# Kernel tuning notes

Hardware: AMD Instinct MI355X
Metric: run time of the kernel (lower is better)

## Reference

```python
import jax, jax.numpy as jnp
import numpy as np

B, T, P, K, R, M = 32, 2048, 128, 256, 8, 64
TAU, TAU_X, TAU_Z = 5, 100.0, 100.0


def _mlp(x, layers):
    # torch nn.Linear: y = x @ W.T + b, each followed by tanh
    for W, b in layers:
        x = jnp.tanh(x @ W.T + b)
    return x


def setup_inputs() -> dict:
    key = jax.random.key(0)
    ks = jax.random.split(key, 24)
    g = lambda k, shp, s=0.1: (jax.random.normal(k, shp, dtype=jnp.float32) * s)
    inp = {
        "in_seq": jax.random.normal(ks[0], (B, T, P), dtype=jnp.float32),
        "L": g(ks[1], (K, R)),
        "Rm": g(ks[2], (K, R)),
        "Wz": g(ks[3], (M, M)),
        "Az_w": g(ks[4], (R, M)),
        "Az_b": jnp.zeros((R,), jnp.float32),
        "ex1_w": g(ks[5], (K, P)), "ex1_b": jnp.zeros((K,), jnp.float32),
        "ex2_w": g(ks[6], (K, K)), "ex2_b": jnp.zeros((K,), jnp.float32),
        "ex3_w": g(ks[7], (K, K)), "ex3_b": jnp.zeros((K,), jnp.float32),
        "ez1_w": g(ks[8], (M, P)), "ez1_b": jnp.zeros((M,), jnp.float32),
        "ez2_w": g(ks[9], (M, M)), "ez2_b": jnp.zeros((M,), jnp.float32),
        "ez3_w": g(ks[10], (M, M)), "ez3_b": jnp.zeros((M,), jnp.float32),
        "de1_w": g(ks[11], (K, K)), "de1_b": jnp.zeros((K,), jnp.float32),
        "de2_w": g(ks[12], (P, K)), "de2_b": jnp.zeros((P,), jnp.float32),
    }
    return inp


def reference(in_seq, L, Rm, Wz, Az_w, Az_b,
              ex1_w, ex1_b, ex2_w, ex2_b, ex3_w, ex3_b,
              ez1_w, ez1_b, ez2_w, ez2_b, ez3_w, ez3_b,
              de1_w, de1_b, de2_w, de2_b):
    enc_x = [(ex1_w, ex1_b), (ex2_w, ex2_b), (ex3_w, ex3_b)]
    enc_z = [(ez1_w, ez1_b), (ez2_w, ez2_b), (ez3_w, ez3_b)]
    dec = [(de1_w, de1_b), (de2_w, de2_b)]

    x_seq = _mlp(in_seq, enc_x)  # [B,T,K]
    z_seq = _mlp(in_seq, enc_z)  # [B,T,M]

    def step(carry, inp):
        x, z = carry          # [B,K], [B,M]
        t, xt, zt = inp       # scalar, [B,K], [B,M]
        # teacher forcing reset every TAU steps (not at t=0)
        reset = (t % TAU == 0) & (t > 0)
        x = jnp.where(reset, xt, x)
        z = jnp.where(reset, zt, z)
        # neuromodulator dynamics
        dz = -z + jnp.tanh(z) @ Wz.T
        z = z + dz / TAU_Z
        s = jax.nn.sigmoid(z @ Az_w.T + Az_b)  # [B,R]
        # low-rank recurrence: bmm(tanh(x), einsum('bir,jr,kr->bijk',s,L,R)[:,0])
        # == ((tanh(x) @ L) * s) @ R.T   (same math, O(K*R) per element)
        dx = -x + ((jnp.tanh(x) @ L) * s) @ Rm.T
        x = x + dx / TAU_X
        x_dec = _mlp(x, dec)  # [B,P]
        return (x, z), (x_dec, z)

    x0 = x_seq[:, 0, :]
    z0 = z_seq[:, 0, :]
    ts = jnp.arange(T)
    xs = jnp.swapaxes(x_seq, 0, 1)  # [T,B,K]
    zs = jnp.swapaxes(z_seq, 0, 1)  # [T,B,M]
    _, (x_pred_t, z_pred_t) = jax.lax.scan(step, (x0, z0), (ts, xs, zs))
    x_pred = jnp.swapaxes(x_pred_t, 0, 1)  # [B,T,P]
    z_pred = jnp.swapaxes(z_pred_t, 0, 1)  # [B,T,M]

    x_recon = _mlp(x_seq, dec)  # [B,T,P]
    return (x_pred, x_recon, z_pred, z_seq)
```

## Files before the change

kernel.cpp:

```cpp
#include <hip/hip_runtime.h>
#include <math.h>

constexpr int B = 32, T = 2048, P = 128, K = 256, R = 8, M = 64;
constexpr int BT = B * T;
constexpr int TAU = 5;
constexpr int NSEG = (T + TAU - 1) / TAU;
constexpr float INV_TAU_X = 1.0f / 100.0f;
constexpr float INV_TAU_Z = 1.0f / 100.0f;

typedef short bf16x4 __attribute__((ext_vector_type(4)));
typedef short bf16x8 __attribute__((ext_vector_type(8)));
typedef float f32x4 __attribute__((ext_vector_type(4)));

static __device__ __forceinline__ short f2bf(float f) {
  unsigned u = __builtin_bit_cast(unsigned, f);
  u += 0x7FFF + ((u >> 16) & 1);
  return (short)(u >> 16);
}
static __device__ __forceinline__ float bf2f(short h) {
  unsigned u = ((unsigned)(unsigned short)h) << 16;
  return __builtin_bit_cast(float, u);
}

static __device__ __forceinline__ float tanh_fast(float x) {
  const float e = __expf(2.f * x);
  return 1.f - 2.f * __builtin_amdgcn_rcpf(e + 1.f);
}
static __device__ __forceinline__ float sigmoid_fast(float x) {
  return __builtin_amdgcn_rcpf(1.f + __expf(-x));
}

static __device__ __forceinline__ void async16(const void* g, void* l) {
  __builtin_amdgcn_global_load_lds(
      (const __attribute__((address_space(1))) void*)g,
      (__attribute__((address_space(3))) void*)l, 16, 0, 0);
}

template <int CTRL>
static __device__ __forceinline__ float dppadd(float p) {
  return p + __builtin_bit_cast(
                 float, __builtin_amdgcn_update_dpp(
                            0, __builtin_bit_cast(int, p), CTRL, 0xF, 0xF, true));
}

static __device__ __forceinline__ void allreduce8(float p[R]) {
#pragma unroll
  for (int r = 0; r < R; ++r) p[r] = dppadd<0xB1>(p[r]);
#pragma unroll
  for (int r = 0; r < R; ++r) p[r] = dppadd<0x4E>(p[r]);
#pragma unroll
  for (int r = 0; r < R; ++r) p[r] = dppadd<0x141>(p[r]);
#pragma unroll
  for (int r = 0; r < R; ++r) p[r] = dppadd<0x140>(p[r]);
#pragma unroll
  for (int r = 0; r < R; ++r)
    p[r] += __builtin_bit_cast(float, __builtin_amdgcn_ds_swizzle(
                                          __builtin_bit_cast(int, p[r]), 0x401F));
#pragma unroll
  for (int r = 0; r < R; ++r)
    p[r] += __shfl_xor(p[r], 32, 64);
}

__global__ __launch_bounds__(256) void split_kernel(
    const float* __restrict__ in, short* __restrict__ h,
    short* __restrict__ l, int n4) {
  const int i = blockIdx.x * 256 + threadIdx.x;
  if (i >= n4) return;
  const float4 v = ((const float4*)in)[i];
  const float f[4] = {v.x, v.y, v.z, v.w};
  bf16x4 ph, pl;
#pragma unroll
  for (int q = 0; q < 4; ++q) {
    ph[q] = f2bf(f[q]);
    pl[q] = f2bf(f[q] - bf2f(ph[q]));
  }
  ((bf16x4*)h)[i] = ph;
  ((bf16x4*)l)[i] = pl;
}

struct W8 {
  const float* src[8];
  unsigned hoff[8];
  unsigned n4[8];
};
__global__ __launch_bounds__(256) void split8_kernel(W8 p, short* __restrict__ dst) {
  const int w = blockIdx.y;
  const int i = blockIdx.x * 256 + threadIdx.x;
  if (i >= (int)p.n4[w]) return;
  const float4 v = ((const float4*)p.src[w])[i];
  const float f[4] = {v.x, v.y, v.z, v.w};
  bf16x4 ph, pl;
#pragma unroll
  for (int q = 0; q < 4; ++q) {
    ph[q] = f2bf(f[q]);
    pl[q] = f2bf(f[q] - bf2f(ph[q]));
  }
  *(bf16x4*)&dst[p.hoff[w] + i * 4] = ph;
  *(bf16x4*)&dst[p.hoff[w] + p.n4[w] * 4 + i * 4] = pl;
}

template <int KIN, int KOUT, int BN, bool SPLIT_OUT>
__global__ __launch_bounds__(256) void gemm_mfma(
    const short* __restrict__ Ah, const short* __restrict__ Al,
    const short* __restrict__ Bh, const short* __restrict__ Bl,
    const float* __restrict__ bias,
    short* __restrict__ Ch, short* __restrict__ Cl,
    float* __restrict__ Cf) {
  constexpr int BK = 64;
  constexpr int WNT = BN / 32;
  constexpr int NB = BN / 8;
  static_assert(KIN % BK == 0, "K tiling");

  __shared__ short AsH[128 * BK];
  __shared__ short AsL[128 * BK];
  __shared__ short BsH[BN * BK];
  __shared__ short BsL[BN * BK];

  const int tid = threadIdx.x;
  const int wave = tid >> 6, lane = tid & 63;
  const int l16 = lane & 15, quad = lane >> 4;
  const int sw = l16 & 7;
  const int warpM = wave & 1, warpN = wave >> 1;
  const int row0 = blockIdx.x * 128;
  const int col0 = blockIdx.y * BN;
  const int srow = lane >> 3;
  const int schunk = (lane & 7) ^ srow;

  f32x4 acc[4][WNT];
#pragma unroll
  for (int i = 0; i < 4; ++i)
#pragma unroll
    for (int j = 0; j < WNT; ++j) acc[i][j] = (f32x4){0.f, 0.f, 0.f, 0.f};

  for (int k0 = 0; k0 < KIN; k0 += BK) {
#pragma unroll
    for (int t = wave; t < 16; t += 4) {
      const size_t goff = (size_t)(row0 + t * 8 + srow) * KIN + k0 + schunk * 8;
      async16(&Ah[goff], &AsH[t * 512]);
      async16(&Al[goff], &AsL[t * 512]);
    }
#pragma unroll
    for (int t = wave; t < NB; t += 4) {
      const size_t goff = (size_t)(col0 + t * 8 + srow) * KIN + k0 + schunk * 8;
      async16(&Bh[goff], &BsH[t * 512]);
      async16(&Bl[goff], &BsL[t * 512]);
    }
    __syncthreads();

#pragma unroll
    for (int kk = 0; kk < 2; ++kk) {
      const int qc = kk * 4 + quad;
      const int qs = (qc ^ sw) * 8;
      bf16x8 ah[4], al[4], bh[WNT], bl[WNT];
#pragma unroll
      for (int i = 0; i < 4; ++i) {
        const int off = (warpM * 64 + i * 16 + l16) * BK + qs;
        ah[i] = *(const bf16x8*)&AsH[off];
        al[i] = *(const bf16x8*)&AsL[off];
      }
#pragma unroll
      for (int j = 0; j < WNT; ++j) {
        const int off = (warpN * WNT * 16 + j * 16 + l16) * BK + qs;
        bh[j] = *(const bf16x8*)&BsH[off];
        bl[j] = *(const bf16x8*)&BsL[off];
      }
#pragma unroll
      for (int i = 0; i < 4; ++i)
#pragma unroll
        for (int j = 0; j < WNT; ++j) {
          acc[i][j] = __builtin_amdgcn_mfma_f32_16x16x32_bf16(ah[i], bh[j],
                                                              acc[i][j], 0, 0, 0);
          acc[i][j] = __builtin_amdgcn_mfma_f32_16x16x32_bf16(al[i], bh[j],
                                                              acc[i][j], 0, 0, 0);
          acc[i][j] = __builtin_amdgcn_mfma_f32_16x16x32_bf16(ah[i], bl[j],
                                                              acc[i][j], 0, 0, 0);
        }
    }
    __syncthreads();
  }

#pragma unroll
  for (int j = 0; j < WNT; ++j) {
    const int col = col0 + warpN * WNT * 16 + j * 16 + l16;
    const float bj = bias[col];
#pragma unroll
    for (int i = 0; i < 4; ++i) {
      const int rbase = row0 + warpM * 64 + i * 16 + quad * 4;
#pragma unroll
      for (int r = 0; r < 4; ++r) {
        const float v = tanh_fast(acc[i][j][r] + bj);
        const size_t idx = (size_t)(rbase + r) * KOUT + col;
        if (SPLIT_OUT) {
          const short h = f2bf(v);
          Ch[idx] = h;
          Cl[idx] = f2bf(v - bf2f(h));
        } else {
          Cf[idx] = v;
        }
      }
    }
  }
}

__global__ __launch_bounds__(512) void scan_kernel(
    const short* xh, const short* xl,
    const float* __restrict__ z_seq,
    const float* __restrict__ Lm, const float* __restrict__ Rm,
    const float* __restrict__ Wz, const float* __restrict__ Az_w,
    const float* __restrict__ Az_b,
    short* xsh, short* xsl,
    float* __restrict__ z_pred) {
  __shared__ __align__(16) float Wz_s[M][68];
  __shared__ __align__(16) float Ls[K * R];
  __shared__ __align__(16) float Rs[K * R];
  __shared__ __align__(16) float tz_s[8][M];

  const int tid = threadIdx.x;
  for (int i = tid; i < M * M; i += 512) Wz_s[i >> 6][i & 63] = Wz[i];
  ((float4*)Ls)[tid] = ((const float4*)Lm)[tid];
  ((float4*)Rs)[tid] = ((const float4*)Rm)[tid];
  __syncthreads();

  const int wave = tid >> 6;
  const int lane = tid & 63;
  const int chain = blockIdx.x * 8 + wave;
  const int b = chain / NSEG;
  const int seg = chain % NSEG;
  const int t0 = seg * TAU;

  float azw[R], azb[R];
#pragma unroll
  for (int r = 0; r < R; ++r) {
    azw[r] = Az_w[r * M + lane];
    azb[r] = Az_b[r];
  }

  float x[4], z;
  {
    const size_t base = ((size_t)b * T + t0);
#pragma unroll
    for (int j = 0; j < 4; ++j)
      x[j] = bf2f(xh[base * K + lane + 64 * j]) + bf2f(xl[base * K + lane + 64 * j]);
    z = z_seq[base * M + lane];
  }

  const float4* wrow = (const float4*)&Wz_s[lane][0];
  const float4* trow = (const float4*)&tz_s[wave][0];

  for (int tt = 0; tt < TAU; ++tt) {
    const int t = t0 + tt;
    const float tz = tanh_fast(z);
    tz_s[wave][lane] = tz;
    float zacc = 0.f;
#pragma unroll
    for (int j = 0; j < 16; ++j) {
      const float4 w = wrow[j], tv = trow[j];
      zacc += w.x * tv.x + w.y * tv.y + w.z * tv.z + w.w * tv.w;
    }
    const float znew = z + (zacc - z) * INV_TAU_Z;

    float s[R];
#pragma unroll
    for (int r = 0; r < R; ++r) s[r] = znew * azw[r];
    allreduce8(s);
#pragma unroll
    for (int r = 0; r < R; ++r) s[r] = sigmoid_fast(s[r] + azb[r]);

    float tx4[4];
#pragma unroll
    for (int j = 0; j < 4; ++j) tx4[j] = tanh_fast(x[j]);
    float v[R];
#pragma unroll
    for (int r = 0; r < R; ++r) v[r] = 0.f;
#pragma unroll
    for (int j = 0; j < 4; ++j) {
      const int kb = (lane + 64 * j) * 8;
      const f32x4 la = *(const f32x4*)&Ls[kb];
      const f32x4 lb = *(const f32x4*)&Ls[kb + 4];
      const float txj = tx4[j];
      v[0] += txj * la[0]; v[1] += txj * la[1];
      v[2] += txj * la[2]; v[3] += txj * la[3];
      v[4] += txj * lb[0]; v[5] += txj * lb[1];
      v[6] += txj * lb[2]; v[7] += txj * lb[3];
    }
    allreduce8(v);
#pragma unroll
    for (int r = 0; r < R; ++r) v[r] *= s[r];
#pragma unroll
    for (int j = 0; j < 4; ++j) {
      const int kb = (lane + 64 * j) * 8;
      const f32x4 ra = *(const f32x4*)&Rs[kb];
      const f32x4 rb = *(const f32x4*)&Rs[kb + 4];
      const float xacc = v[0] * ra[0] + v[1] * ra[1] + v[2] * ra[2] +
                         v[3] * ra[3] + v[4] * rb[0] + v[5] * rb[1] +
                         v[6] * rb[2] + v[7] * rb[3];
      x[j] = x[j] + (xacc - x[j]) * INV_TAU_X;
    }

    if (t < T) {
      const size_t o = ((size_t)b * T + t);
#pragma unroll
      for (int j = 0; j < 4; ++j) {
        const short h = f2bf(x[j]);
        xsh[o * K + lane + 64 * j] = h;
        xsl[o * K + lane + 64 * j] = f2bf(x[j] - bf2f(h));
      }
      z_pred[o * M + lane] = znew;
    }
    z = znew;
  }
}

extern "C" void kernel_launch(void* const* d_in, const int* in_sizes, int n_in,
                              void* d_out, int out_size, void* d_ws,
                              size_t ws_size, hipStream_t stream) {
  const float* in_seq = (const float*)d_in[0];
  const float* Lm    = (const float*)d_in[1];
  const float* Rm    = (const float*)d_in[2];
  const float* Wz    = (const float*)d_in[3];
  const float* Az_w  = (const float*)d_in[4];
  const float* Az_b  = (const float*)d_in[5];
  const float* ex1_w = (const float*)d_in[6];
  const float* ex1_b = (const float*)d_in[7];
  const float* ex2_w = (const float*)d_in[8];
  const float* ex2_b = (const float*)d_in[9];
  const float* ex3_w = (const float*)d_in[10];
  const float* ex3_b = (const float*)d_in[11];
  const float* ez1_w = (const float*)d_in[12];
  const float* ez1_b = (const float*)d_in[13];
  const float* ez2_w = (const float*)d_in[14];
  const float* ez2_b = (const float*)d_in[15];
  const float* ez3_w = (const float*)d_in[16];
  const float* ez3_b = (const float*)d_in[17];
  const float* de1_w = (const float*)d_in[18];
  const float* de1_b = (const float*)d_in[19];
  const float* de2_w = (const float*)d_in[20];
  const float* de2_b = (const float*)d_in[21];

  float* out = (float*)d_out;
  float* x_pred  = out;
  float* x_recon = out + (size_t)BT * P;
  float* z_pred  = out + (size_t)2 * BT * P;
  float* z_seq   = out + (size_t)2 * BT * P + (size_t)BT * M;

  short* S0h = (short*)d_ws;
  short* S0l = S0h + (size_t)BT * K;
  short* S1h = S0l + (size_t)BT * K;
  short* S1l = S1h + (size_t)BT * K;
  short* Z0h = S1h;
  short* Z0l = S1h + (size_t)BT * M;
  short* Z1h = S1h + (size_t)2 * BT * M;
  short* Z1l = S1h + (size_t)3 * BT * M;
  short* INh = (short*)x_pred;
  short* INl = INh + (size_t)BT * P;
  short* Wr  = (short*)z_pred;
  short* WD1 = (short*)x_pred;
  short* WD2 = (short*)d_ws;

  const unsigned HO_EX1 = 0,      HO_EX2 = 65536,  HO_EX3 = 196608;
  const unsigned HO_DE1 = 327680, HO_DE2 = 458752;
  const unsigned HO_EZ1 = 524288, HO_EZ2 = 540672, HO_EZ3 = 548864;

  const dim3 blk(256);
  const dim3 gx(BT / 128, 2);
  const dim3 g128(BT / 128, 1);
  const dim3 g64(BT / 128, 1);

  split_kernel<<<dim3(BT * P / 4 / 256), blk, 0, stream>>>(in_seq, INh, INl, BT * P / 4);
  W8 w8;
  w8.src[0] = ex1_w; w8.hoff[0] = HO_EX1; w8.n4[0] = 8192;
  w8.src[1] = ex2_w; w8.hoff[1] = HO_EX2; w8.n4[1] = 16384;
  w8.src[2] = ex3_w; w8.hoff[2] = HO_EX3; w8.n4[2] = 16384;
  w8.src[3] = de1_w; w8.hoff[3] = HO_DE1; w8.n4[3] = 16384;
  w8.src[4] = de2_w; w8.hoff[4] = HO_DE2; w8.n4[4] = 8192;
  w8.src[5] = ez1_w; w8.hoff[5] = HO_EZ1; w8.n4[5] = 2048;
  w8.src[6] = ez2_w; w8.hoff[6] = HO_EZ2; w8.n4[6] = 1024;
  w8.src[7] = ez3_w; w8.hoff[7] = HO_EZ3; w8.n4[7] = 1024;
  split8_kernel<<<dim3(64, 8), blk, 0, stream>>>(w8, Wr);

  gemm_mfma<128, 256, 128, true><<<gx, blk, 0, stream>>>(
      INh, INl, Wr + HO_EX1, Wr + HO_EX1 + 32768, ex1_b, S0h, S0l, nullptr);
  gemm_mfma<256, 256, 128, true><<<gx, blk, 0, stream>>>(
      S0h, S0l, Wr + HO_EX2, Wr + HO_EX2 + 65536, ex2_b, S1h, S1l, nullptr);
  gemm_mfma<256, 256, 128, true><<<gx, blk, 0, stream>>>(
      S1h, S1l, Wr + HO_EX3, Wr + HO_EX3 + 65536, ex3_b, S0h, S0l, nullptr);
  gemm_mfma<256, 256, 128, true><<<gx, blk, 0, stream>>>(
      S0h, S0l, Wr + HO_DE1, Wr + HO_DE1 + 65536, de1_b, S1h, S1l, nullptr);
  gemm_mfma<256, 128, 128, false><<<g128, blk, 0, stream>>>(
      S1h, S1l, Wr + HO_DE2, Wr + HO_DE2 + 32768, de2_b, nullptr, nullptr, x_recon);
  gemm_mfma<128, 64, 64, true><<<g64, blk, 0, stream>>>(
      INh, INl, Wr + HO_EZ1, Wr + HO_EZ1 + 8192, ez1_b, Z0h, Z0l, nullptr);
  gemm_mfma<64, 64, 64, true><<<g64, blk, 0, stream>>>(
      Z0h, Z0l, Wr + HO_EZ2, Wr + HO_EZ2 + 4096, ez2_b, Z1h, Z1l, nullptr);
  gemm_mfma<64, 64, 64, false><<<g64, blk, 0, stream>>>(
      Z1h, Z1l, Wr + HO_EZ3, Wr + HO_EZ3 + 4096, ez3_b, nullptr, nullptr, z_seq);
  split_kernel<<<dim3(64), blk, 0, stream>>>(de1_w, WD1, WD1 + 65536, 16384);
  scan_kernel<<<dim3(B * NSEG / 8), dim3(512), 0, stream>>>(
      S0h, S0l, z_seq, Lm, Rm, Wz, Az_w, Az_b, S0h, S0l, z_pred);
  gemm_mfma<256, 256, 128, true><<<gx, blk, 0, stream>>>(
      S0h, S0l, WD1, WD1 + 65536, de1_b, S1h, S1l, nullptr);
  split_kernel<<<dim3(32), blk, 0, stream>>>(de2_w, WD2, WD2 + 32768, 8192);
  gemm_mfma<256, 128, 128, false><<<g128, blk, 0, stream>>>(
      S1h, S1l, WD2, WD2 + 32768, de2_b, nullptr, nullptr, x_pred);
}
```

Baseline: 542.8 us.

## Double-buffer GEMM shared-memory tiles with BK=32 and prefetch next tile

The split-bf16 MFMA GEMM now halves the K tile to 32 and keeps two shared-memory buffers. The global-to-LDS async copy for the next K tile is issued before the current tile's MFMA work, so the load can overlap compute. The swizzle pattern is adjusted to fit the narrower tile. This raises the number of K iterations and barriers per tile, and the async copies still need a wait before their data is consumed.

```diff
diff --git a/kernel.cpp b/kernel.cpp
--- a/kernel.cpp
+++ b/kernel.cpp
@@ -106,25 +106,26 @@
     const float* __restrict__ bias,
     short* __restrict__ Ch, short* __restrict__ Cl,
     float* __restrict__ Cf) {
-  constexpr int BK = 64;
+  constexpr int BK = 32;
   constexpr int WNT = BN / 32;
-  constexpr int NB = BN / 8;
+  constexpr int AW = 128 / 16;
+  constexpr int BW = BN / 16;
   static_assert(KIN % BK == 0, "K tiling");
 
-  __shared__ short AsH[128 * BK];
-  __shared__ short AsL[128 * BK];
-  __shared__ short BsH[BN * BK];
-  __shared__ short BsL[BN * BK];
+  __shared__ short AsH[2][128 * BK];
+  __shared__ short AsL[2][128 * BK];
+  __shared__ short BsH[2][BN * BK];
+  __shared__ short BsL[2][BN * BK];
 
   const int tid = threadIdx.x;
   const int wave = tid >> 6, lane = tid & 63;
   const int l16 = lane & 15, quad = lane >> 4;
-  const int sw = l16 & 7;
   const int warpM = wave & 1, warpN = wave >> 1;
   const int row0 = blockIdx.x * 128;
   const int col0 = blockIdx.y * BN;
-  const int srow = lane >> 3;
-  const int schunk = (lane & 7) ^ srow;
+  const int srow = lane >> 2;
+  const int schunk = (lane & 3) ^ ((lane >> 3) & 3);
+  const int rdslot = (quad ^ ((l16 >> 1) & 3)) * 8;
 
   f32x4 acc[4][WNT];
 #pragma unroll
@@ -132,50 +133,62 @@
 #pragma unroll
     for (int j = 0; j < WNT; ++j) acc[i][j] = (f32x4){0.f, 0.f, 0.f, 0.f};
 
+#pragma unroll
+  for (int t = wave; t < AW; t += 4) {
+    const size_t goff = (size_t)(row0 + t * 16 + srow) * KIN + schunk * 8;
+    async16(&Ah[goff], &AsH[0][t * 512]);
+    async16(&Al[goff], &AsL[0][t * 512]);
+  }
+#pragma unroll
+  for (int t = wave; t < BW; t += 4) {
+    const size_t goff = (size_t)(col0 + t * 16 + srow) * KIN + schunk * 8;
+    async16(&Bh[goff], &BsH[0][t * 512]);
+    async16(&Bl[goff], &BsL[0][t * 512]);
+  }
+  __syncthreads();
+
   for (int k0 = 0; k0 < KIN; k0 += BK) {
-#pragma unroll
-    for (int t = wave; t < 16; t += 4) {
-      const size_t goff = (size_t)(row0 + t * 8 + srow) * KIN + k0 + schunk * 8;
-      async16(&Ah[goff], &AsH[t * 512]);
-      async16(&Al[goff], &AsL[t * 512]);
-    }
-#pragma unroll
-    for (int t = wave; t < NB; t += 4) {
-      const size_t goff = (size_t)(col0 + t * 8 + srow) * KIN + k0 + schunk * 8;
-      async16(&Bh[goff], &BsH[t * 512]);
-      async16(&Bl[goff], &BsL[t * 512]);
-    }
-    __syncthreads();
-
-#pragma unroll
-    for (int kk = 0; kk < 2; ++kk) {
-      const int qc = kk * 4 + quad;
-      const int qs = (qc ^ sw) * 8;
-      bf16x8 ah[4], al[4], bh[WNT], bl[WNT];
-#pragma unroll
-      for (int i = 0; i < 4; ++i) {
-        const int off = (warpM * 64 + i * 16 + l16) * BK + qs;
-        ah[i] = *(const bf16x8*)&AsH[off];
-        al[i] = *(const bf16x8*)&AsL[off];
+    const int cur = (k0 >> 5) & 1;
+    if (k0 + BK < KIN) {
+      const int nxt = cur ^ 1;
+      const int kn = k0 + BK;
+#pragma unroll
+      for (int t = wave; t < AW; t += 4) {
+        const size_t goff = (size_t)(row0 + t * 16 + srow) * KIN + kn + schunk * 8;
+        async16(&Ah[goff], &AsH[nxt][t * 512]);
+        async16(&Al[goff], &AsL[nxt][t * 512]);
       }
 #pragma unroll
+      for (int t = wave; t < BW; t += 4) {
+        const size_t goff = (size_t)(col0 + t * 16 + srow) * KIN + kn + schunk * 8;
+        async16(&Bh[goff], &BsH[nxt][t * 512]);
+        async16(&Bl[goff], &BsL[nxt][t * 512]);
+      }
+    }
+    bf16x8 ah[4], al[4], bh[WNT], bl[WNT];
+#pragma unroll
+    for (int i = 0; i < 4; ++i) {
+      const int off = (warpM * 64 + i * 16 + l16) * BK + rdslot;
+      ah[i] = *(const bf16x8*)&AsH[cur][off];
+      al[i] = *(const bf16x8*)&AsL[cur][off];
+    }
+#pragma unroll
+    for (int j = 0; j < WNT; ++j) {
+      const int off = (warpN * WNT * 16 + j * 16 + l16) * BK + rdslot;
+      bh[j] = *(const bf16x8*)&BsH[cur][off];
+      bl[j] = *(const bf16x8*)&BsL[cur][off];
+    }
+#pragma unroll
+    for (int i = 0; i < 4; ++i)
+#pragma unroll
       for (int j = 0; j < WNT; ++j) {
-        const int off = (warpN * WNT * 16 + j * 16 + l16) * BK + qs;
-        bh[j] = *(const bf16x8*)&BsH[off];
-        bl[j] = *(const bf16x8*)&BsL[off];
+        acc[i][j] = __builtin_amdgcn_mfma_f32_16x16x32_bf16(ah[i], bh[j],
+                                                            acc[i][j], 0, 0, 0);
+        acc[i][j] = __builtin_amdgcn_mfma_f32_16x16x32_bf16(al[i], bh[j],
+                                                            acc[i][j], 0, 0, 0);
+        acc[i][j] = __builtin_amdgcn_mfma_f32_16x16x32_bf16(ah[i], bl[j],
+                                                            acc[i][j], 0, 0, 0);
       }
-#pragma unroll
-      for (int i = 0; i < 4; ++i)
-#pragma unroll
-        for (int j = 0; j < WNT; ++j) {
-          acc[i][j] = __builtin_amdgcn_mfma_f32_16x16x32_bf16(ah[i], bh[j],
-                                                              acc[i][j], 0, 0, 0);
-          acc[i][j] = __builtin_amdgcn_mfma_f32_16x16x32_bf16(al[i], bh[j],
-                                                              acc[i][j], 0, 0, 0);
-          acc[i][j] = __builtin_amdgcn_mfma_f32_16x16x32_bf16(ah[i], bl[j],
-                                                              acc[i][j], 0, 0, 0);
-        }
-    }
     __syncthreads();
   }
 
```

Measured after the change: 576.4 us. +6.2%, slower.

## Replace LDS-staged split-bf16 GEMM with register-direct fp32-input GEMM

Applied to the files above, without the earlier changes.

Activations between MLP layers are now stored as fp32 instead of hi/lo bf16 pairs. The GEMM loads A and B fragments directly from global memory into registers, with no LDS staging, and splits A to hi/lo bf16 on the fly. The input split kernel is removed and the scan kernel now reads and writes fp32 x. This saves the split pass and the LDS barriers. In exchange it loses LDS tile reuse: each wave reloads B from global/L2 and every A element is reconverted per tile.

```diff
diff --git a/kernel.cpp b/kernel.cpp
--- a/kernel.cpp
+++ b/kernel.cpp
@@ -28,12 +28,6 @@
 }
 static __device__ __forceinline__ float sigmoid_fast(float x) {
   return __builtin_amdgcn_rcpf(1.f + __expf(-x));
-}
-
-static __device__ __forceinline__ void async16(const void* g, void* l) {
-  __builtin_amdgcn_global_load_lds(
-      (const __attribute__((address_space(1))) void*)g,
-      (__attribute__((address_space(3))) void*)l, 16, 0, 0);
 }
 
 template <int CTRL>
@@ -99,32 +93,20 @@
   *(bf16x4*)&dst[p.hoff[w] + p.n4[w] * 4 + i * 4] = pl;
 }
 
-template <int KIN, int KOUT, int BN, bool SPLIT_OUT>
-__global__ __launch_bounds__(256) void gemm_mfma(
-    const short* __restrict__ Ah, const short* __restrict__ Al,
-    const short* __restrict__ Bh, const short* __restrict__ Bl,
-    const float* __restrict__ bias,
-    short* __restrict__ Ch, short* __restrict__ Cl,
-    float* __restrict__ Cf) {
-  constexpr int BK = 64;
+template <int KIN, int KOUT, int BN>
+__global__ __launch_bounds__(256, 2) void gemm_reg(
+    const float* __restrict__ A, const short* __restrict__ Bh,
+    const short* __restrict__ Bl, const float* __restrict__ bias,
+    float* __restrict__ C) {
   constexpr int WNT = BN / 32;
-  constexpr int NB = BN / 8;
-  static_assert(KIN % BK == 0, "K tiling");
-
-  __shared__ short AsH[128 * BK];
-  __shared__ short AsL[128 * BK];
-  __shared__ short BsH[BN * BK];
-  __shared__ short BsL[BN * BK];
+  static_assert(KIN % 32 == 0, "K tiling");
 
   const int tid = threadIdx.x;
   const int wave = tid >> 6, lane = tid & 63;
   const int l16 = lane & 15, quad = lane >> 4;
-  const int sw = l16 & 7;
   const int warpM = wave & 1, warpN = wave >> 1;
-  const int row0 = blockIdx.x * 128;
-  const int col0 = blockIdx.y * BN;
-  const int srow = lane >> 3;
-  const int schunk = (lane & 7) ^ srow;
+  const int row0 = blockIdx.x * 128 + warpM * 64;
+  const int col0 = blockIdx.y * BN + warpN * WNT * 16;
 
   f32x4 acc[4][WNT];
 #pragma unroll
@@ -132,83 +114,71 @@
 #pragma unroll
     for (int j = 0; j < WNT; ++j) acc[i][j] = (f32x4){0.f, 0.f, 0.f, 0.f};
 
-  for (int k0 = 0; k0 < KIN; k0 += BK) {
-#pragma unroll
-    for (int t = wave; t < 16; t += 4) {
-      const size_t goff = (size_t)(row0 + t * 8 + srow) * KIN + k0 + schunk * 8;
-      async16(&Ah[goff], &AsH[t * 512]);
-      async16(&Al[goff], &AsL[t * 512]);
-    }
-#pragma unroll
-    for (int t = wave; t < NB; t += 4) {
-      const size_t goff = (size_t)(col0 + t * 8 + srow) * KIN + k0 + schunk * 8;
-      async16(&Bh[goff], &BsH[t * 512]);
-      async16(&Bl[goff], &BsL[t * 512]);
-    }
-    __syncthreads();
-
-#pragma unroll
-    for (int kk = 0; kk < 2; ++kk) {
-      const int qc = kk * 4 + quad;
-      const int qs = (qc ^ sw) * 8;
-      bf16x8 ah[4], al[4], bh[WNT], bl[WNT];
-#pragma unroll
-      for (int i = 0; i < 4; ++i) {
-        const int off = (warpM * 64 + i * 16 + l16) * BK + qs;
-        ah[i] = *(const bf16x8*)&AsH[off];
-        al[i] = *(const bf16x8*)&AsL[off];
+  const float* arow[4];
+#pragma unroll
+  for (int i = 0; i < 4; ++i)
+    arow[i] = A + (size_t)(row0 + i * 16 + l16) * KIN + quad * 8;
+  const short* bch[WNT];
+  const short* bcl[WNT];
+#pragma unroll
+  for (int j = 0; j < WNT; ++j) {
+    const size_t off = (size_t)(col0 + j * 16 + l16) * KIN + quad * 8;
+    bch[j] = Bh + off;
+    bcl[j] = Bl + off;
+  }
+
+#pragma unroll 2
+  for (int k0 = 0; k0 < KIN; k0 += 32) {
+    bf16x8 bh[WNT], bl[WNT];
+#pragma unroll
+    for (int j = 0; j < WNT; ++j) {
+      bh[j] = *(const bf16x8*)(bch[j] + k0);
+      bl[j] = *(const bf16x8*)(bcl[j] + k0);
+    }
+#pragma unroll
+    for (int i = 0; i < 4; ++i) {
+      const f32x4 a0 = *(const f32x4*)(arow[i] + k0);
+      const f32x4 a1 = *(const f32x4*)(arow[i] + k0 + 4);
+      bf16x8 ah, al;
+#pragma unroll
+      for (int e = 0; e < 4; ++e) {
+        ah[e] = f2bf(a0[e]);
+        al[e] = f2bf(a0[e] - bf2f(ah[e]));
+        ah[4 + e] = f2bf(a1[e]);
+        al[4 + e] = f2bf(a1[e] - bf2f(ah[4 + e]));
       }
 #pragma unroll
       for (int j = 0; j < WNT; ++j) {
-        const int off = (warpN * WNT * 16 + j * 16 + l16) * BK + qs;
-        bh[j] = *(const bf16x8*)&BsH[off];
-        bl[j] = *(const bf16x8*)&BsL[off];
+        acc[i][j] = __builtin_amdgcn_mfma_f32_16x16x32_bf16(ah, bh[j],
+                                                            acc[i][j], 0, 0, 0);
+        acc[i][j] = __builtin_amdgcn_mfma_f32_16x16x32_bf16(al, bh[j],
+                                                            acc[i][j], 0, 0, 0);
+        acc[i][j] = __builtin_amdgcn_mfma_f32_16x16x32_bf16(ah, bl[j],
+                                                            acc[i][j], 0, 0, 0);
       }
-#pragma unroll
-      for (int i = 0; i < 4; ++i)
-#pragma unroll
-        for (int j = 0; j < WNT; ++j) {
-          acc[i][j] = __builtin_amdgcn_mfma_f32_16x16x32_bf16(ah[i], bh[j],
-                                                              acc[i][j], 0, 0, 0);
-          acc[i][j] = __builtin_amdgcn_mfma_f32_16x16x32_bf16(al[i], bh[j],
-                                                              acc[i][j], 0, 0, 0);
-          acc[i][j] = __builtin_amdgcn_mfma_f32_16x16x32_bf16(ah[i], bl[j],
-                                                              acc[i][j], 0, 0, 0);
-        }
-    }
-    __syncthreads();
+    }
   }
 
 #pragma unroll
   for (int j = 0; j < WNT; ++j) {
-    const int col = col0 + warpN * WNT * 16 + j * 16 + l16;
+    const int col = col0 + j * 16 + l16;
     const float bj = bias[col];
 #pragma unroll
     for (int i = 0; i < 4; ++i) {
-      const int rbase = row0 + warpM * 64 + i * 16 + quad * 4;
-#pragma unroll
-      for (int r = 0; r < 4; ++r) {
-        const float v = tanh_fast(acc[i][j][r] + bj);
-        const size_t idx = (size_t)(rbase + r) * KOUT + col;
-        if (SPLIT_OUT) {
-          const short h = f2bf(v);
-          Ch[idx] = h;
-          Cl[idx] = f2bf(v - bf2f(h));
-        } else {
-          Cf[idx] = v;
-        }
-      }
+      const int rbase = row0 + i * 16 + quad * 4;
+#pragma unroll
+      for (int r = 0; r < 4; ++r)
+        C[(size_t)(rbase + r) * KOUT + col] = tanh_fast(acc[i][j][r] + bj);
     }
   }
 }
 
 __global__ __launch_bounds__(512) void scan_kernel(
-    const short* xh, const short* xl,
+    float* xs,
     const float* __restrict__ z_seq,
     const float* __restrict__ Lm, const float* __restrict__ Rm,
     const float* __restrict__ Wz, const float* __restrict__ Az_w,
     const float* __restrict__ Az_b,
-    short* xsh, short* xsl,
     float* __restrict__ z_pred) {
   __shared__ __align__(16) float Wz_s[M][68];
   __shared__ __align__(16) float Ls[K * R];
@@ -239,8 +209,7 @@
   {
     const size_t base = ((size_t)b * T + t0);
 #pragma unroll
-    for (int j = 0; j < 4; ++j)
-      x[j] = bf2f(xh[base * K + lane + 64 * j]) + bf2f(xl[base * K + lane + 64 * j]);
+    for (int j = 0; j < 4; ++j) x[j] = xs[base * K + lane + 64 * j];
     z = z_seq[base * M + lane];
   }
 
@@ -300,11 +269,7 @@
     if (t < T) {
       const size_t o = ((size_t)b * T + t);
 #pragma unroll
-      for (int j = 0; j < 4; ++j) {
-        const short h = f2bf(x[j]);
-        xsh[o * K + lane + 64 * j] = h;
-        xsl[o * K + lane + 64 * j] = f2bf(x[j] - bf2f(h));
-      }
+      for (int j = 0; j < 4; ++j) xs[o * K + lane + 64 * j] = x[j];
       z_pred[o * M + lane] = znew;
     }
     z = znew;
@@ -343,19 +308,13 @@
   float* z_pred  = out + (size_t)2 * BT * P;
   float* z_seq   = out + (size_t)2 * BT * P + (size_t)BT * M;
 
-  short* S0h = (short*)d_ws;
-  short* S0l = S0h + (size_t)BT * K;
-  short* S1h = S0l + (size_t)BT * K;
-  short* S1l = S1h + (size_t)BT * K;
-  short* Z0h = S1h;
-  short* Z0l = S1h + (size_t)BT * M;
-  short* Z1h = S1h + (size_t)2 * BT * M;
-  short* Z1l = S1h + (size_t)3 * BT * M;
-  short* INh = (short*)x_pred;
-  short* INl = INh + (size_t)BT * P;
+  float* X0 = (float*)d_ws;
+  float* X1 = X0 + (size_t)BT * K;
+  float* Z0 = X1;
+  float* Z1 = X1 + (size_t)BT * M;
   short* Wr  = (short*)z_pred;
   short* WD1 = (short*)x_pred;
-  short* WD2 = (short*)d_ws;
+  short* WD2 = (short*)X0;
 
   const unsigned HO_EX1 = 0,      HO_EX2 = 65536,  HO_EX3 = 196608;
   const unsigned HO_DE1 = 327680, HO_DE2 = 458752;
@@ -366,7 +325,6 @@
   const dim3 g128(BT / 128, 1);
   const dim3 g64(BT / 128, 1);
 
-  split_kernel<<<dim3(BT * P / 4 / 256), blk, 0, stream>>>(in_seq, INh, INl, BT * P / 4);
   W8 w8;
   w8.src[0] = ex1_w; w8.hoff[0] = HO_EX1; w8.n4[0] = 8192;
   w8.src[1] = ex2_w; w8.hoff[1] = HO_EX2; w8.n4[1] = 16384;
@@ -378,28 +336,28 @@
   w8.src[7] = ez3_w; w8.hoff[7] = HO_EZ3; w8.n4[7] = 1024;
   split8_kernel<<<dim3(64, 8), blk, 0, stream>>>(w8, Wr);
 
-  gemm_mfma<128, 256, 128, true><<<gx, blk, 0, stream>>>(
-      INh, INl, Wr + HO_EX1, Wr + HO_EX1 + 32768, ex1_b, S0h, S0l, nullptr);
-  gemm_mfma<256, 256, 128, true><<<gx, blk, 0, stream>>>(
-      S0h, S0l, Wr + HO_EX2, Wr + HO_EX2 + 65536, ex2_b, S1h, S1l, nullptr);
-  gemm_mfma<256, 256, 128, true><<<gx, blk, 0, stream>>>(
-      S1h, S1l, Wr + HO_EX3, Wr + HO_EX3 + 65536, ex3_b, S0h, S0l, nullptr);
-  gemm_mfma<256, 256, 128, true><<<gx, blk, 0, stream>>>(
-      S0h, S0l, Wr + HO_DE1, Wr + HO_DE1 + 65536, de1_b, S1h, S1l, nullptr);
-  gemm_mfma<256, 128, 128, false><<<g128, blk, 0, stream>>>(
-      S1h, S1l, Wr + HO_DE2, Wr + HO_DE2 + 32768, de2_b, nullptr, nullptr, x_recon);
-  gemm_mfma<128, 64, 64, true><<<g64, blk, 0, stream>>>(
-      INh, INl, Wr + HO_EZ1, Wr + HO_EZ1 + 8192, ez1_b, Z0h, Z0l, nullptr);
-  gemm_mfma<64, 64, 64, true><<<g64, blk, 0, stream>>>(
-      Z0h, Z0l, Wr + HO_EZ2, Wr + HO_EZ2 + 4096, ez2_b, Z1h, Z1l, nullptr);
-  gemm_mfma<64, 64, 64, false><<<g64, blk, 0, stream>>>(
-      Z1h, Z1l, Wr + HO_EZ3, Wr + HO_EZ3 + 4096, ez3_b, nullptr, nullptr, z_seq);
+  gemm_reg<128, 256, 128><<<gx, blk, 0, stream>>>(
+      in_seq, Wr + HO_EX1, Wr + HO_EX1 + 32768, ex1_b, X0);
+  gemm_reg<256, 256, 128><<<gx, blk, 0, stream>>>(
+      X0, Wr + HO_EX2, Wr + HO_EX2 + 65536, ex2_b, X1);
+  gemm_reg<256, 256, 128><<<gx, blk, 0, stream>>>(
+      X1, Wr + HO_EX3, Wr + HO_EX3 + 65536, ex3_b, X0);
+  gemm_reg<256, 256, 128><<<gx, blk, 0, stream>>>(
+      X0, Wr + HO_DE1, Wr + HO_DE1 + 65536, de1_b, X1);
+  gemm_reg<256, 128, 128><<<g128, blk, 0, stream>>>(
+      X1, Wr + HO_DE2, Wr + HO_DE2 + 32768, de2_b, x_recon);
+  gemm_reg<128, 64, 64><<<g64, blk, 0, stream>>>(
+      in_seq, Wr + HO_EZ1, Wr + HO_EZ1 + 8192, ez1_b, Z0);
+  gemm_reg<64, 64, 64><<<g64, blk, 0, stream>>>(
+      Z0, Wr + HO_EZ2, Wr + HO_EZ2 + 4096, ez2_b, Z1);
+  gemm_reg<64, 64, 64><<<g64, blk, 0, stream>>>(
+      Z1, Wr + HO_EZ3, Wr + HO_EZ3 + 4096, ez3_b, z_seq);
   split_kernel<<<dim3(64), blk, 0, stream>>>(de1_w, WD1, WD1 + 65536, 16384);
   scan_kernel<<<dim3(B * NSEG / 8), dim3(512), 0, stream>>>(
-      S0h, S0l, z_seq, Lm, Rm, Wz, Az_w, Az_b, S0h, S0l, z_pred);
-  gemm_mfma<256, 256, 128, true><<<gx, blk, 0, stream>>>(
-      S0h, S0l, WD1, WD1 + 65536, de1_b, S1h, S1l, nullptr);
+      X0, z_seq, Lm, Rm, Wz, Az_w, Az_b, z_pred);
+  gemm_reg<256, 256, 128><<<gx, blk, 0, stream>>>(
+      X0, WD1, WD1 + 65536, de1_b, X1);
   split_kernel<<<dim3(32), blk, 0, stream>>>(de2_w, WD2, WD2 + 32768, 8192);
-  gemm_mfma<256, 128, 128, false><<<g128, blk, 0, stream>>>(
-      S1h, S1l, WD2, WD2 + 32768, de2_b, nullptr, nullptr, x_pred);
-}
+  gemm_reg<256, 128, 128><<<g128, blk, 0, stream>>>(
+      X1, WD2, WD2 + 32768, de2_b, x_pred);
+}
```

New measurement: 669.3 us. 1.23x slower.
